# Kernel tuning notes

Measured on AMD Instinct MI355X. Metric: run time of the kernel, lower is better.

Reference implementation:

```python
import jax, jax.numpy as jnp
import numpy as np

TOP_K = 2

def setup_inputs() -> dict:
    key = jax.random.key(0)
    ks = jax.random.split(key, 5)
    N, D, E, H, O = 2048, 1024, 16, 2048, 1024
    s_in = 1.0 / np.sqrt(D)
    s_h = 1.0 / np.sqrt(H)
    return {
        "z": jax.random.normal(ks[0], (N, D), dtype=jnp.float32),
        "router_w": jax.random.normal(ks[1], (E, D), dtype=jnp.float32) * s_in,
        "router_b": jnp.zeros((E,), dtype=jnp.float32),
        "w1": jax.random.normal(ks[2], (E, H, D), dtype=jnp.float32) * s_in,
        "b1": jnp.zeros((E, H), dtype=jnp.float32),
        "w2": jax.random.normal(ks[3], (E, O, H), dtype=jnp.float32) * s_h,
        "b2": jnp.zeros((E, O), dtype=jnp.float32),
    }

def reference(z, router_w, router_b, w1, b1, w2, b2):
    # Router: softmax over experts, then top-k with renormalized weights
    logits = z @ router_w.T + router_b                      # [N, E]
    probs = jax.nn.softmax(logits, axis=-1)                 # [N, E]
    topk_prob, topk_idx = jax.lax.top_k(probs, TOP_K)       # [N, K]
    topk_prob = topk_prob / topk_prob.sum(axis=-1, keepdims=True)

    # Dense all-expert MLP (faithful to original mix(): every expert on every token)
    h = jax.nn.gelu(jnp.einsum('nd,ehd->neh', z, w1) + b1, approximate=False)  # [N, E, H]
    expert_out = jnp.einsum('neh,eoh->neo', h, w2) + b2                        # [N, E, O]

    # Gather top-k expert outputs and combine with routing weights
    picked = jnp.take_along_axis(expert_out, topk_idx[:, :, None], axis=1)     # [N, K, O]
    return (picked * topk_prob[:, :, None]).sum(axis=1)                        # [N, O]
```

## Files before the change

### kernel.cpp

```cpp
#include <hip/hip_runtime.h>
#include <hip/hip_bf16.h>
#include <math.h>

#define N_TOK 2048
#define DIM   1024
#define NE    16
#define NH    2048
#define NO    1024

typedef __attribute__((ext_vector_type(8))) short short8;
typedef __attribute__((ext_vector_type(4))) float f32x4;

__device__ __forceinline__ unsigned short f2bf(float f) {
  union { float f; unsigned u; } v; v.f = f;
  unsigned r = v.u + 0x7FFFu + ((v.u >> 16) & 1u);
  return (unsigned short)(r >> 16);
}

__device__ __forceinline__ short8 pack8(float4 a, float4 b) {
  short8 r;
  r[0] = (short)f2bf(a.x); r[1] = (short)f2bf(a.y);
  r[2] = (short)f2bf(a.z); r[3] = (short)f2bf(a.w);
  r[4] = (short)f2bf(b.x); r[5] = (short)f2bf(b.y);
  r[6] = (short)f2bf(b.z); r[7] = (short)f2bf(b.w);
  return r;
}

__global__ __launch_bounds__(256) void router_kernel(
    const float* __restrict__ z, const float* __restrict__ rw,
    const float* __restrict__ rb, int* __restrict__ counts,
    int* __restrict__ list, float* __restrict__ tkw) {
  const int n = blockIdx.x;
  const int t = threadIdx.x;
  const int e = t >> 4, sub = t & 15;
  const float* zr = z + (size_t)n * DIM;
  const float* wr = rw + (size_t)e * DIM;
  double acc = 0.0;
#pragma unroll
  for (int i = 0; i < 16; ++i) {
    const int d = i * 64 + sub * 4;
    const float4 zv = *(const float4*)(zr + d);
    const float4 wv = *(const float4*)(wr + d);
    acc += (double)zv.x * wv.x + (double)zv.y * wv.y
         + (double)zv.z * wv.z + (double)zv.w * wv.w;
  }
  acc += __shfl_xor(acc, 8, 16);
  acc += __shfl_xor(acc, 4, 16);
  acc += __shfl_xor(acc, 2, 16);
  acc += __shfl_xor(acc, 1, 16);
  __shared__ double logits[NE];
  if (sub == 0) logits[e] = acc + (double)rb[e];
  __syncthreads();
  if (t == 0) {
    int i0 = -1, i1 = -1; double v0 = -1e300, v1 = -1e300;
    for (int i = 0; i < NE; ++i) {
      const double v = logits[i];
      if (v > v0) { v1 = v0; i1 = i0; v0 = v; i0 = i; }
      else if (v > v1) { v1 = v; i1 = i; }
    }
    const double w0 = 1.0 / (1.0 + exp(v1 - v0));
    tkw[n * 2 + 0] = (float)w0;
    tkw[n * 2 + 1] = (float)(1.0 - w0);
    const int p0 = atomicAdd(&counts[i0], 1); list[i0 * N_TOK + p0] = n * 2;
    const int p1 = atomicAdd(&counts[i1], 1); list[i1 * N_TOK + p1] = n * 2 + 1;
  }
}

#define BM 128
#define BN 64
#define BK 64
#define LDK 72
#define NNT1 (NH / BN)
#define NNT2 (NO / BN)

__global__ __launch_bounds__(256, 4) void gemm1_kernel(
    const float* __restrict__ z, const float* __restrict__ w1,
    const float* __restrict__ b1, const int* __restrict__ counts,
    const int* __restrict__ list, unsigned short* __restrict__ h) {
  const int bid = blockIdx.x;
  const int mt  = bid / (NE * NNT1);
  const int rem = bid - mt * (NE * NNT1);
  const int e   = rem >> 5;
  const int nt  = rem & 31;
  const int ne = counts[e];
  if (mt * BM >= ne) return;
  const int t = threadIdx.x;

  __shared__ unsigned short As[BM][LDK];
  __shared__ unsigned short Bs[BN][LDK];
  __shared__ int ent[BM];
  if (t < BM) {
    const int idx = mt * BM + t;
    ent[t] = (idx < ne) ? list[e * N_TOK + idx] : -1;
  }
  __syncthreads();

  const int lane = t & 63, wave = t >> 6;
  const int wm = (wave & 1) * 64, wn = (wave >> 1) * 32;
  const int l15 = lane & 15, q8 = (lane >> 4) * 8;

  f32x4 acc[4][2];
#pragma unroll
  for (int i = 0; i < 4; ++i)
#pragma unroll
    for (int j = 0; j < 2; ++j) acc[i][j] = (f32x4){0.f, 0.f, 0.f, 0.f};

  const int row8 = t >> 3;
  const int col8 = (t & 7) * 8;

  const float* aR[4];
  const float* bR[2];
  const float* bbase = w1 + ((size_t)e * NH + (size_t)nt * BN) * DIM;
#pragma unroll
  for (int p = 0; p < 4; ++p) {
    const int en = ent[row8 + p * 32];
    aR[p] = z + (size_t)(en >= 0 ? (en >> 1) : 0) * DIM + col8;
  }
#pragma unroll
  for (int p = 0; p < 2; ++p) bR[p] = bbase + (size_t)(row8 + p * 32) * DIM + col8;

  float4 va[4][2], vb[2][2];
#pragma unroll
  for (int p = 0; p < 4; ++p) { va[p][0] = *(const float4*)(aR[p]); va[p][1] = *(const float4*)(aR[p] + 4); }
#pragma unroll
  for (int p = 0; p < 2; ++p) { vb[p][0] = *(const float4*)(bR[p]); vb[p][1] = *(const float4*)(bR[p] + 4); }

  for (int k0 = 0; k0 < DIM; k0 += BK) {
#pragma unroll
    for (int p = 0; p < 4; ++p)
      *(short8*)&As[row8 + p * 32][col8] = pack8(va[p][0], va[p][1]);
#pragma unroll
    for (int p = 0; p < 2; ++p)
      *(short8*)&Bs[row8 + p * 32][col8] = pack8(vb[p][0], vb[p][1]);
    __syncthreads();
    if (k0 + BK < DIM) {
      const int kn = k0 + BK;
#pragma unroll
      for (int p = 0; p < 4; ++p) { va[p][0] = *(const float4*)(aR[p] + kn); va[p][1] = *(const float4*)(aR[p] + kn + 4); }
#pragma unroll
      for (int p = 0; p < 2; ++p) { vb[p][0] = *(const float4*)(bR[p] + kn); vb[p][1] = *(const float4*)(bR[p] + kn + 4); }
    }
#pragma unroll
    for (int kk = 0; kk < BK; kk += 32) {
      short8 a[4], b[2];
#pragma unroll
      for (int i = 0; i < 4; ++i) a[i] = *(const short8*)&As[wm + i * 16 + l15][kk + q8];
#pragma unroll
      for (int j = 0; j < 2; ++j) b[j] = *(const short8*)&Bs[wn + j * 16 + l15][kk + q8];
#pragma unroll
      for (int i = 0; i < 4; ++i)
#pragma unroll
        for (int j = 0; j < 2; ++j)
          acc[i][j] = __builtin_amdgcn_mfma_f32_16x16x32_bf16(a[i], b[j], acc[i][j], 0, 0, 0);
    }
    __syncthreads();
  }

  const int r4 = (lane >> 4) * 4;
#pragma unroll
  for (int i = 0; i < 4; ++i) {
#pragma unroll
    for (int reg = 0; reg < 4; ++reg) {
      const int row = wm + i * 16 + r4 + reg;
      const int en = ent[row];
      if (en < 0) continue;
      unsigned short* hrow = h + (size_t)en * NH;
#pragma unroll
      for (int j = 0; j < 2; ++j) {
        const int col = nt * BN + wn + j * 16 + l15;
        float v = acc[i][j][reg] + b1[e * NH + col];
        v = 0.5f * v * (1.0f + erff(v * 0.70710678118654752f));
        hrow[col] = f2bf(v);
      }
    }
  }
}

__global__ __launch_bounds__(256, 4) void gemm2_kernel(
    const unsigned short* __restrict__ h, const float* __restrict__ w2,
    const float* __restrict__ b2, const int* __restrict__ counts,
    const int* __restrict__ list, float* __restrict__ contrib) {
  const int bid = blockIdx.x;
  const int mt  = bid >> 8;
  const int e   = (bid >> 4) & 15;
  const int nt  = bid & 15;
  const int ne = counts[e];
  if (mt * BM >= ne) return;
  const int t = threadIdx.x;

  __shared__ unsigned short As[BM][LDK];
  __shared__ unsigned short Bs[BN][LDK];
  __shared__ int ent[BM];
  if (t < BM) {
    const int idx = mt * BM + t;
    ent[t] = (idx < ne) ? list[e * N_TOK + idx] : -1;
  }
  __syncthreads();

  const int lane = t & 63, wave = t >> 6;
  const int wm = (wave & 1) * 64, wn = (wave >> 1) * 32;
  const int l15 = lane & 15, q8 = (lane >> 4) * 8;

  f32x4 acc[4][2];
#pragma unroll
  for (int i = 0; i < 4; ++i)
#pragma unroll
    for (int j = 0; j < 2; ++j) acc[i][j] = (f32x4){0.f, 0.f, 0.f, 0.f};

  const int row8 = t >> 3;
  const int col8 = (t & 7) * 8;

  const unsigned short* aR[4];
#pragma unroll
  for (int p = 0; p < 4; ++p) {
    const int en = ent[row8 + p * 32];
    aR[p] = h + (size_t)(en >= 0 ? en : 0) * NH + col8;
  }
  const float* bR[2];
  const float* bbase = w2 + ((size_t)e * NO + (size_t)nt * BN) * NH;
#pragma unroll
  for (int p = 0; p < 2; ++p) bR[p] = bbase + (size_t)(row8 + p * 32) * NH + col8;

  float4 va[4], vb[2][2];
#pragma unroll
  for (int p = 0; p < 4; ++p) va[p] = *(const float4*)(aR[p]);
#pragma unroll
  for (int p = 0; p < 2; ++p) { vb[p][0] = *(const float4*)(bR[p]); vb[p][1] = *(const float4*)(bR[p] + 4); }

  for (int k0 = 0; k0 < NH; k0 += BK) {
#pragma unroll
    for (int p = 0; p < 4; ++p)
      *(float4*)&As[row8 + p * 32][col8] = va[p];
#pragma unroll
    for (int p = 0; p < 2; ++p)
      *(short8*)&Bs[row8 + p * 32][col8] = pack8(vb[p][0], vb[p][1]);
    __syncthreads();
    if (k0 + BK < NH) {
      const int kn = k0 + BK;
#pragma unroll
      for (int p = 0; p < 4; ++p) va[p] = *(const float4*)(aR[p] + kn);
#pragma unroll
      for (int p = 0; p < 2; ++p) { vb[p][0] = *(const float4*)(bR[p] + kn); vb[p][1] = *(const float4*)(bR[p] + kn + 4); }
    }
#pragma unroll
    for (int kk = 0; kk < BK; kk += 32) {
      short8 a[4], b[2];
#pragma unroll
      for (int i = 0; i < 4; ++i) a[i] = *(const short8*)&As[wm + i * 16 + l15][kk + q8];
#pragma unroll
      for (int j = 0; j < 2; ++j) b[j] = *(const short8*)&Bs[wn + j * 16 + l15][kk + q8];
#pragma unroll
      for (int i = 0; i < 4; ++i)
#pragma unroll
        for (int j = 0; j < 2; ++j)
          acc[i][j] = __builtin_amdgcn_mfma_f32_16x16x32_bf16(a[i], b[j], acc[i][j], 0, 0, 0);
    }
    __syncthreads();
  }

  const int r4 = (lane >> 4) * 4;
#pragma unroll
  for (int i = 0; i < 4; ++i) {
#pragma unroll
    for (int reg = 0; reg < 4; ++reg) {
      const int row = wm + i * 16 + r4 + reg;
      const int en = ent[row];
      if (en < 0) continue;
      float* crow = contrib + (size_t)en * NO;
#pragma unroll
      for (int j = 0; j < 2; ++j) {
        const int col = nt * BN + wn + j * 16 + l15;
        crow[col] = acc[i][j][reg] + b2[e * NO + col];
      }
    }
  }
}

__global__ __launch_bounds__(256) void combine_kernel(
    const float* __restrict__ contrib, const float* __restrict__ tkw,
    float* __restrict__ out) {
  const int gid = blockIdx.x * 256 + threadIdx.x;
  const int n = gid >> 8;
  const int c = (gid & 255) * 4;
  const float w0 = tkw[n * 2], w1 = tkw[n * 2 + 1];
  const float4 a = *(const float4*)(contrib + (size_t)(n * 2) * NO + c);
  const float4 b = *(const float4*)(contrib + (size_t)(n * 2 + 1) * NO + c);
  float4 o;
  o.x = w0 * a.x + w1 * b.x; o.y = w0 * a.y + w1 * b.y;
  o.z = w0 * a.z + w1 * b.z; o.w = w0 * a.w + w1 * b.w;
  *(float4*)(out + (size_t)n * NO + c) = o;
}

extern "C" void kernel_launch(void* const* d_in, const int* in_sizes, int n_in,
                              void* d_out, int out_size, void* d_ws, size_t ws_size,
                              hipStream_t stream) {
  const float* z  = (const float*)d_in[0];
  const float* rw = (const float*)d_in[1];
  const float* rb = (const float*)d_in[2];
  const float* w1 = (const float*)d_in[3];
  const float* b1 = (const float*)d_in[4];
  const float* w2 = (const float*)d_in[5];
  const float* b2 = (const float*)d_in[6];
  float* out = (float*)d_out;

  char* ws = (char*)d_ws;
  int*   counts = (int*)ws;
  int*   list   = (int*)(ws + 256);
  float* tkw    = (float*)(ws + 256 + 131072);
  unsigned short* h = (unsigned short*)(ws + 262144);
  float* contrib = (float*)(ws + 262144 + 16777216);

  hipMemsetAsync(counts, 0, NE * sizeof(int), stream);
  router_kernel<<<N_TOK, 256, 0, stream>>>(z, rw, rb, counts, list, tkw);
  gemm1_kernel<<<16 * NE * NNT1, 256, 0, stream>>>(z, w1, b1, counts, list, h);
  gemm2_kernel<<<16 * NE * NNT2, 256, 0, stream>>>(h, w2, b2, counts, list, contrib);
  combine_kernel<<<(N_TOK * (NO / 4)) / 256, 256, 0, stream>>>(contrib, tkw, out);
}
```

Baseline: 507.4 us.

## Use LDS-only barriers in GEMM loops and remap block order for busy tiles

```diff
diff --git a/kernel.cpp b/kernel.cpp
--- a/kernel.cpp
+++ b/kernel.cpp
@@ -24,6 +24,11 @@
   r[4] = (short)f2bf(b.x); r[5] = (short)f2bf(b.y);
   r[6] = (short)f2bf(b.z); r[7] = (short)f2bf(b.w);
   return r;
+}
+
+__device__ __forceinline__ void lds_barrier() {
+  __builtin_amdgcn_s_waitcnt(0xC07F);
+  __builtin_amdgcn_s_barrier();
 }
 
 __global__ __launch_bounds__(256) void router_kernel(
@@ -73,25 +78,35 @@
 #define NNT1 (NH / BN)
 #define NNT2 (NO / BN)
 
+__device__ __forceinline__ void decode_bid(int bid, int nent, int& mt, int& ent) {
+  if (bid < 2 * nent) {
+    mt = (bid >> 3) & 1;
+    ent = (bid >> 4) * 8 + (bid & 7);
+  } else {
+    const int t2 = bid - 2 * nent;
+    mt = 2 + t2 / nent;
+    ent = t2 - (mt - 2) * nent;
+  }
+}
+
 __global__ __launch_bounds__(256, 4) void gemm1_kernel(
     const float* __restrict__ z, const float* __restrict__ w1,
     const float* __restrict__ b1, const int* __restrict__ counts,
     const int* __restrict__ list, unsigned short* __restrict__ h) {
-  const int bid = blockIdx.x;
-  const int mt  = bid / (NE * NNT1);
-  const int rem = bid - mt * (NE * NNT1);
-  const int e   = rem >> 5;
-  const int nt  = rem & 31;
+  int mt, ent;
+  decode_bid(blockIdx.x, NE * NNT1, mt, ent);
+  const int e  = ent >> 5;
+  const int nt = ent & 31;
   const int ne = counts[e];
   if (mt * BM >= ne) return;
   const int t = threadIdx.x;
 
   __shared__ unsigned short As[BM][LDK];
   __shared__ unsigned short Bs[BN][LDK];
-  __shared__ int ent[BM];
+  __shared__ int ent_s[BM];
   if (t < BM) {
     const int idx = mt * BM + t;
-    ent[t] = (idx < ne) ? list[e * N_TOK + idx] : -1;
+    ent_s[t] = (idx < ne) ? list[e * N_TOK + idx] : -1;
   }
   __syncthreads();
 
@@ -113,7 +128,7 @@
   const float* bbase = w1 + ((size_t)e * NH + (size_t)nt * BN) * DIM;
 #pragma unroll
   for (int p = 0; p < 4; ++p) {
-    const int en = ent[row8 + p * 32];
+    const int en = ent_s[row8 + p * 32];
     aR[p] = z + (size_t)(en >= 0 ? (en >> 1) : 0) * DIM + col8;
   }
 #pragma unroll
@@ -132,7 +147,7 @@
 #pragma unroll
     for (int p = 0; p < 2; ++p)
       *(short8*)&Bs[row8 + p * 32][col8] = pack8(vb[p][0], vb[p][1]);
-    __syncthreads();
+    lds_barrier();
     if (k0 + BK < DIM) {
       const int kn = k0 + BK;
 #pragma unroll
@@ -153,7 +168,7 @@
         for (int j = 0; j < 2; ++j)
           acc[i][j] = __builtin_amdgcn_mfma_f32_16x16x32_bf16(a[i], b[j], acc[i][j], 0, 0, 0);
     }
-    __syncthreads();
+    lds_barrier();
   }
 
   const int r4 = (lane >> 4) * 4;
@@ -162,7 +177,7 @@
 #pragma unroll
     for (int reg = 0; reg < 4; ++reg) {
       const int row = wm + i * 16 + r4 + reg;
-      const int en = ent[row];
+      const int en = ent_s[row];
       if (en < 0) continue;
       unsigned short* hrow = h + (size_t)en * NH;
 #pragma unroll
@@ -180,20 +195,20 @@
     const unsigned short* __restrict__ h, const float* __restrict__ w2,
     const float* __restrict__ b2, const int* __restrict__ counts,
     const int* __restrict__ list, float* __restrict__ contrib) {
-  const int bid = blockIdx.x;
-  const int mt  = bid >> 8;
-  const int e   = (bid >> 4) & 15;
-  const int nt  = bid & 15;
+  int mt, ent;
+  decode_bid(blockIdx.x, NE * NNT2, mt, ent);
+  const int e  = ent >> 4;
+  const int nt = ent & 15;
   const int ne = counts[e];
   if (mt * BM >= ne) return;
   const int t = threadIdx.x;
 
   __shared__ unsigned short As[BM][LDK];
   __shared__ unsigned short Bs[BN][LDK];
-  __shared__ int ent[BM];
+  __shared__ int ent_s[BM];
   if (t < BM) {
     const int idx = mt * BM + t;
-    ent[t] = (idx < ne) ? list[e * N_TOK + idx] : -1;
+    ent_s[t] = (idx < ne) ? list[e * N_TOK + idx] : -1;
   }
   __syncthreads();
 
@@ -213,7 +228,7 @@
   const unsigned short* aR[4];
 #pragma unroll
   for (int p = 0; p < 4; ++p) {
-    const int en = ent[row8 + p * 32];
+    const int en = ent_s[row8 + p * 32];
     aR[p] = h + (size_t)(en >= 0 ? en : 0) * NH + col8;
   }
   const float* bR[2];
@@ -234,7 +249,7 @@
 #pragma unroll
     for (int p = 0; p < 2; ++p)
       *(short8*)&Bs[row8 + p * 32][col8] = pack8(vb[p][0], vb[p][1]);
-    __syncthreads();
+    lds_barrier();
     if (k0 + BK < NH) {
       const int kn = k0 + BK;
 #pragma unroll
@@ -255,7 +270,7 @@
         for (int j = 0; j < 2; ++j)
           acc[i][j] = __builtin_amdgcn_mfma_f32_16x16x32_bf16(a[i], b[j], acc[i][j], 0, 0, 0);
     }
-    __syncthreads();
+    lds_barrier();
   }
 
   const int r4 = (lane >> 4) * 4;
@@ -264,7 +279,7 @@
 #pragma unroll
     for (int reg = 0; reg < 4; ++reg) {
       const int row = wm + i * 16 + r4 + reg;
-      const int en = ent[row];
+      const int en = ent_s[row];
       if (en < 0) continue;
       float* crow = contrib + (size_t)en * NO;
 #pragma unroll
```

Measured after the change: 497.4 us. 1.02x faster.
